# Kernel tuning notes

Measured on AMD Instinct MI355X. Metric: run time of the kernel, lower is better.

The kernel has to match this reference:

```python
import jax, jax.numpy as jnp
import numpy as np
import math

D_MODEL = 1024
N_HEADS = 16
D_K = D_MODEL // N_HEADS
NB_FEATURES = max(1, math.ceil(math.log(D_MODEL)))  # 7
D_FF = 4096
BH = 4  # block_size_h
BW = 4  # block_size_w
EPS_LN = 1e-6


def gelu_approx(x):
    c = math.sqrt(2.0 / math.pi)
    return 0.5 * x * (1.0 + jnp.tanh(c * (x + 0.044715 * x * x * x)))


def layer_norm(x, alpha, bias):
    # torch .std() uses ddof=1 (unbiased)
    mean = x.mean(axis=-1, keepdims=True)
    std = jnp.std(x, axis=-1, ddof=1, keepdims=True)
    return alpha * (x - mean) / (std + EPS_LN) + bias


def causal_performer(q_in, k_in, v_in, wq, wk, wv, wo, omega):
    B, Sq, D = q_in.shape
    Sk = k_in.shape[1]
    q = (q_in @ wq.T).reshape(B, Sq, N_HEADS, D_K)
    k = (k_in @ wk.T).reshape(B, Sk, N_HEADS, D_K)
    v = (v_in @ wv.T).reshape(B, Sk, N_HEADS, D_K)
    # exp kernel feature map: exp(-0.5 * (x @ omega^T)^2)
    qp = jnp.exp(-0.5 * jnp.square(q @ omega.T))  # (B,Sq,H,nb)
    kp = jnp.exp(-0.5 * jnp.square(k @ omega.T))  # (B,Sk,H,nb)
    qp = qp / (qp.sum(-1, keepdims=True) + 1e-6)
    kp = kp / (kp.sum(-1, keepdims=True) + 1e-6)
    K_cum = jnp.cumsum(kp, axis=1)                               # (B,Sk,H,nb)
    KV_cum = jnp.cumsum(kp[..., None] * v[..., None, :], axis=1)  # (B,Sk,H,nb,dk)
    key_idx = jnp.clip((jnp.arange(Sq) // BH + 1) * BW - 1, None, Sk - 1)
    K_sel = K_cum[:, key_idx]    # (B,Sq,H,nb)
    KV_sel = KV_cum[:, key_idx]  # (B,Sq,H,nb,dk)
    num = jnp.einsum('bshn,bshnd->bshd', qp, KV_sel)
    den = jnp.einsum('bshn,bshn->bsh', qp, K_sel)[..., None]
    out = (num / (den + 1e-6)).reshape(B, Sq, D)
    return out @ wo.T


def setup_inputs() -> dict:
    key = jax.random.key(0)
    ks = jax.random.split(key, 24)
    s = 0.02
    p = {}
    p['x'] = jax.random.normal(ks[0], (2, 4096, D_MODEL), jnp.float32)
    p['lto'] = jax.random.normal(ks[1], (2, 4096, D_MODEL), jnp.float32)
    for i, nm in enumerate(['wq_s', 'wk_s', 'wv_s', 'wo_s']):
        p[nm] = jax.random.normal(ks[2 + i], (D_MODEL, D_MODEL), jnp.float32) * s
    for i, nm in enumerate(['wq_c', 'wk_c', 'wv_c', 'wo_c']):
        p[nm] = jax.random.normal(ks[6 + i], (D_MODEL, D_MODEL), jnp.float32) * s
    p['omega_s'] = jax.random.normal(ks[10], (NB_FEATURES, D_K), jnp.float32) / math.sqrt(D_K)
    p['omega_c'] = jax.random.normal(ks[11], (NB_FEATURES, D_K), jnp.float32) / math.sqrt(D_K)
    p['w1'] = jax.random.normal(ks[12], (D_FF, D_MODEL), jnp.float32) * s
    p['b1'] = jnp.zeros((D_FF,), jnp.float32)
    p['w2'] = jax.random.normal(ks[13], (D_MODEL, D_FF), jnp.float32) * s
    p['b2'] = jnp.zeros((D_MODEL,), jnp.float32)
    for i in range(3):
        p[f'ln{i}_a'] = jnp.ones((D_MODEL,), jnp.float32)
        p[f'ln{i}_b'] = jnp.zeros((D_MODEL,), jnp.float32)
    return p


def reference(x, lto, wq_s, wk_s, wv_s, wo_s, wq_c, wk_c, wv_c, wo_c,
              omega_s, omega_c, w1, b1, w2, b2,
              ln0_a, ln0_b, ln1_a, ln1_b, ln2_a, ln2_b):
    # residual 0: self-attention on x
    xn = layer_norm(x, ln0_a, ln0_b)
    x = x + causal_performer(xn, xn, xn, wq_s, wk_s, wv_s, wo_s, omega_s)
    # residual 1: cross-attention, queries = normed lto, keys/values = updated x
    ln = layer_norm(lto, ln1_a, ln1_b)
    lto = lto + causal_performer(ln, x, x, wq_c, wk_c, wv_c, wo_c, omega_c)
    # residual 2: feed-forward
    fn = layer_norm(lto, ln2_a, ln2_b)
    ff = gelu_approx(fn @ w1.T + b1) @ w2.T + b2
    return lto + ff
```

## Files before the change

kernel.cpp:

```cpp
#include <hip/hip_runtime.h>
#include <cstdint>
#include <cstddef>

typedef __bf16 bf16;
typedef __bf16 bf16x8 __attribute__((ext_vector_type(8)));
typedef __bf16 bf16x4 __attribute__((ext_vector_type(4)));
typedef float  f32x4  __attribute__((ext_vector_type(4)));

#define NB 7
static constexpr int Bq = 2, Sq = 4096, Dm = 1024, Dff = 4096;
static constexpr int Mrows = Bq * Sq;
static constexpr int NCH = Sq / 4;
static constexpr int CSW = 464;

__device__ __forceinline__ void gload16(const void* g, void* l) {
  __builtin_amdgcn_global_load_lds((__attribute__((address_space(1))) void*)g,
                                   (__attribute__((address_space(3))) void*)l,
                                   16, 0, 0);
}

template <int N> __device__ __forceinline__ void wait_vmcnt() {
  asm volatile("s_waitcnt vmcnt(%0)" :: "n"(N) : "memory");
}
__device__ __forceinline__ void wait_lgkm0() {
  asm volatile("s_waitcnt lgkmcnt(0)" ::: "memory");
}
__device__ __forceinline__ void sbar() {
  __builtin_amdgcn_sched_barrier(0);
  __builtin_amdgcn_s_barrier();
  __builtin_amdgcn_sched_barrier(0);
}

__device__ __forceinline__ float gelu_f(float x) {
  const float c = 0.79788456080286535588f;
  float z = c * (x + 0.044715f * x * x * x);
  float t = 1.f - 2.f / (__expf(2.f * z) + 1.f);
  return 0.5f * x * (1.f + t);
}

struct CvtA {
  const float* s[10];
  bf16* d[10];
  int start[11];
};
__global__ __launch_bounds__(256) void cvt10(CvtA a) {
  const int i = blockIdx.x * 256 + threadIdx.x;
  int r = 0;
#pragma unroll
  for (int k = 1; k < 10; ++k) r += (i >= a.start[k]);
  const int o = i - a.start[r];
  f32x4 v = *(const f32x4*)&a.s[r][(size_t)o * 4];
  bf16x4 ov;
#pragma unroll
  for (int e = 0; e < 4; ++e) ov[e] = (bf16)v[e];
  *(bf16x4*)&a.d[r][(size_t)o * 4] = ov;
}

__global__ __launch_bounds__(256) void ln_kernel(const float* __restrict__ x,
                                                 const float* __restrict__ alpha,
                                                 const float* __restrict__ beta,
                                                 bf16* __restrict__ out) {
  const int row = blockIdx.x, tid = threadIdx.x;
  const float* xr = x + (size_t)row * Dm;
  f32x4 v = *(const f32x4*)&xr[tid * 4];
  float s  = v[0] + v[1] + v[2] + v[3];
  float s2 = v[0]*v[0] + v[1]*v[1] + v[2]*v[2] + v[3]*v[3];
#pragma unroll
  for (int o = 32; o > 0; o >>= 1) { s += __shfl_xor(s, o); s2 += __shfl_xor(s2, o); }
  __shared__ float red[8];
  const int wid = tid >> 6, lane = tid & 63;
  if (lane == 0) { red[wid] = s; red[wid + 4] = s2; }
  __syncthreads();
  s  = red[0] + red[1] + red[2] + red[3];
  s2 = red[4] + red[5] + red[6] + red[7];
  const float mean = s * (1.f / 1024.f);
  float var = (s2 - s * mean) * (1.f / 1023.f);
  var = fmaxf(var, 0.f);
  const float inv = 1.f / (sqrtf(var) + 1e-6f);
  f32x4 a4 = *(const f32x4*)&alpha[tid * 4];
  f32x4 b4 = *(const f32x4*)&beta[tid * 4];
  bf16x4 o4;
#pragma unroll
  for (int e = 0; e < 4; ++e) o4[e] = (bf16)(a4[e] * (v[e] - mean) * inv + b4[e]);
  *(bf16x4*)&out[(size_t)row * Dm + tid * 4] = o4;
}

template <int MODE>
__global__ __launch_bounds__(512, 2) void gemm256(
    const bf16* __restrict__ A, const bf16* __restrict__ Bw,
    int M, int N, int K,
    const float* __restrict__ bias, const float* __restrict__ res,
    float* __restrict__ outF, bf16* __restrict__ outB) {
  constexpr int BM = 256, BN = 256;
  constexpr int ACH = 4, LPT = 8, MFR = 8, MH = 4;
  __shared__ __align__(16) bf16 As[2][BM * 64];
  __shared__ __align__(16) bf16 Bs[2][BN * 64];

  const int tid = threadIdx.x;
  const int lane = tid & 63, wid = tid >> 6;
  const int wm = wid >> 2, wn = wid & 3;

  int bid = blockIdx.x;
  const int nwg = gridDim.x;
  bid = (bid & 7) * (nwg >> 3) + (bid >> 3);
  const int nbx = N / BN;
  const int bm = (bid / nbx) * BM, bn = (bid % nbx) * BN;
  const int NT = K >> 6;

  const int srow = tid >> 3;
  const int scol = ((tid & 7) ^ (srow & 7)) * 8;
  const bf16* Ag = A  + (size_t)(bm + srow) * K + scol;
  const bf16* Bg = Bw + (size_t)(bn + srow) * K + scol;

  f32x4 acc[MFR][4] = {};
  const int lr = lane & 15, uo = lane >> 4;

  auto stA = [&](int buf, int t) {
#pragma unroll
    for (int c = 0; c < ACH; ++c)
      gload16(Ag + ((size_t)(c * 64) * K + (size_t)t * 64),
              (char*)(&As[buf][0]) + c * 8192 + wid * 1024);
  };
  auto stB = [&](int buf, int t) {
#pragma unroll
    for (int c = 0; c < 4; ++c)
      gload16(Bg + ((size_t)(c * 64) * K + (size_t)t * 64),
              (char*)(&Bs[buf][0]) + c * 8192 + wid * 1024);
  };

  stA(0, 0); stB(0, 0);
  stA(1, 1); stB(1, 1);
  wait_vmcnt<LPT>();
  sbar();

  bf16x8 a0[MH][2], a1[MH][2], b0[2][2], b1[2][2];

  for (int t = 0; t < NT; ++t) {
    const int cur = t & 1;
    const bf16* Asb = &As[cur][0];
    const bf16* Bsb = &Bs[cur][0];

#pragma unroll
    for (int i = 0; i < MH; ++i)
#pragma unroll
      for (int kh = 0; kh < 2; ++kh) {
        const int r = wm * (BM / 2) + i * 16 + lr;
        const int u = (kh * 4 + uo) ^ (lr & 7);
        a0[i][kh] = *(const bf16x8*)&Asb[r * 64 + u * 8];
      }
#pragma unroll
    for (int j = 0; j < 2; ++j)
#pragma unroll
      for (int kh = 0; kh < 2; ++kh) {
        const int r = wn * 64 + j * 16 + lr;
        const int u = (kh * 4 + uo) ^ (lr & 7);
        b0[j][kh] = *(const bf16x8*)&Bsb[r * 64 + u * 8];
      }
    __builtin_amdgcn_sched_barrier(0);
    __builtin_amdgcn_s_barrier();
    wait_lgkm0();
    __builtin_amdgcn_sched_barrier(0);
    __builtin_amdgcn_s_setprio(1);
#pragma unroll
    for (int i = 0; i < MH; ++i)
#pragma unroll
      for (int j = 0; j < 2; ++j) {
        acc[i][j] = __builtin_amdgcn_mfma_f32_16x16x32_bf16(a0[i][0], b0[j][0], acc[i][j], 0, 0, 0);
        acc[i][j] = __builtin_amdgcn_mfma_f32_16x16x32_bf16(a0[i][1], b0[j][1], acc[i][j], 0, 0, 0);
      }
    __builtin_amdgcn_s_setprio(0);
    sbar();

#pragma unroll
    for (int j = 0; j < 2; ++j)
#pragma unroll
      for (int kh = 0; kh < 2; ++kh) {
        const int r = wn * 64 + (2 + j) * 16 + lr;
        const int u = (kh * 4 + uo) ^ (lr & 7);
        b1[j][kh] = *(const bf16x8*)&Bsb[r * 64 + u * 8];
      }
    __builtin_amdgcn_sched_barrier(0);
    __builtin_amdgcn_s_barrier();
    wait_lgkm0();
    __builtin_amdgcn_sched_barrier(0);
    __builtin_amdgcn_s_setprio(1);
#pragma unroll
    for (int i = 0; i < MH; ++i)
#pragma unroll
      for (int j = 0; j < 2; ++j) {
        acc[i][2 + j] = __builtin_amdgcn_mfma_f32_16x16x32_bf16(a0[i][0], b1[j][0], acc[i][2 + j], 0, 0, 0);
        acc[i][2 + j] = __builtin_amdgcn_mfma_f32_16x16x32_bf16(a0[i][1], b1[j][1], acc[i][2 + j], 0, 0, 0);
      }
    __builtin_amdgcn_s_setprio(0);
    sbar();

#pragma unroll
    for (int i = 0; i < MH; ++i)
#pragma unroll
      for (int kh = 0; kh < 2; ++kh) {
        const int r = wm * (BM / 2) + (MH + i) * 16 + lr;
        const int u = (kh * 4 + uo) ^ (lr & 7);
        a1[i][kh] = *(const bf16x8*)&Asb[r * 64 + u * 8];
      }
    __builtin_amdgcn_sched_barrier(0);
    if (t + 2 < NT) stB(cur, t + 2);
    __builtin_amdgcn_sched_barrier(0);
    __builtin_amdgcn_s_barrier();
    wait_lgkm0();
    __builtin_amdgcn_sched_barrier(0);
    __builtin_amdgcn_s_setprio(1);
#pragma unroll
    for (int i = 0; i < MH; ++i)
#pragma unroll
      for (int j = 0; j < 2; ++j) {
        acc[MH + i][2 + j] = __builtin_amdgcn_mfma_f32_16x16x32_bf16(a1[i][0], b1[j][0], acc[MH + i][2 + j], 0, 0, 0);
        acc[MH + i][2 + j] = __builtin_amdgcn_mfma_f32_16x16x32_bf16(a1[i][1], b1[j][1], acc[MH + i][2 + j], 0, 0, 0);
      }
    __builtin_amdgcn_s_setprio(0);
    sbar();

    if (t + 2 < NT) stA(cur, t + 2);
    __builtin_amdgcn_sched_barrier(0);
    __builtin_amdgcn_s_barrier();
    __builtin_amdgcn_sched_barrier(0);
    __builtin_amdgcn_s_setprio(1);
#pragma unroll
    for (int i = 0; i < MH; ++i)
#pragma unroll
      for (int j = 0; j < 2; ++j) {
        acc[MH + i][j] = __builtin_amdgcn_mfma_f32_16x16x32_bf16(a1[i][0], b0[j][0], acc[MH + i][j], 0, 0, 0);
        acc[MH + i][j] = __builtin_amdgcn_mfma_f32_16x16x32_bf16(a1[i][1], b0[j][1], acc[MH + i][j], 0, 0, 0);
      }
    __builtin_amdgcn_s_setprio(0);
    __builtin_amdgcn_sched_barrier(0);
    if (t < NT - 2) wait_vmcnt<LPT>();
    else            wait_vmcnt<0>();
    __builtin_amdgcn_s_barrier();
    __builtin_amdgcn_sched_barrier(0);
  }

#pragma unroll
  for (int f = 0; f < MFR; ++f) {
    const int r0 = bm + wm * (BM / 2) + f * 16 + (lane >> 4) * 4;
#pragma unroll
    for (int g = 0; g < 4; ++g) {
      const int c = bn + wn * 64 + g * 16 + (lane & 15);
      float bv = 0.f;
      if (MODE == 3) bv = bias[c];
#pragma unroll
      for (int r = 0; r < 4; ++r) {
        const size_t idx = (size_t)(r0 + r) * N + c;
        float v = acc[f][g][r];
        if (MODE == 3) v = gelu_f(v + bv);
        outB[idx] = (bf16)v;
      }
    }
  }
}

template <int MODE>
__global__ __launch_bounds__(512, 2) void gemm128(
    const bf16* __restrict__ A, const bf16* __restrict__ Bw,
    int M, int N, int K,
    const float* __restrict__ bias, const float* __restrict__ res,
    float* __restrict__ outF, bf16* __restrict__ outB) {
  constexpr int BM = 128, BN = 256;
  __shared__ __align__(16) bf16 As[3][BM * 64];
  __shared__ __align__(16) bf16 Bs[3][BN * 64];

  const int tid = threadIdx.x;
  const int lane = tid & 63, wid = tid >> 6;
  const int wm = wid >> 2, wn = wid & 3;

  int bid = blockIdx.x;
  const int nwg = gridDim.x;
  bid = (bid & 7) * (nwg >> 3) + (bid >> 3);
  const int nbx = N / BN;
  const int bm = (bid / nbx) * BM, bn = (bid % nbx) * BN;
  const int NT = K >> 6;

  const int srow = tid >> 3;
  const int scol = ((tid & 7) ^ (srow & 7)) * 8;
  const bf16* Ag = A  + (size_t)(bm + srow) * K + scol;
  const bf16* Bg = Bw + (size_t)(bn + srow) * K + scol;

  f32x4 acc[4][4] = {};
  const int lr = lane & 15, uo = lane >> 4;

  auto stA = [&](int buf, int t) {
#pragma unroll
    for (int c = 0; c < 2; ++c)
      gload16(Ag + ((size_t)(c * 64) * K + (size_t)t * 64),
              (char*)(&As[buf][0]) + c * 8192 + wid * 1024);
  };
  auto stB = [&](int buf, int t) {
#pragma unroll
    for (int c = 0; c < 4; ++c)
      gload16(Bg + ((size_t)(c * 64) * K + (size_t)t * 64),
              (char*)(&Bs[buf][0]) + c * 8192 + wid * 1024);
  };

  stA(0, 0); stB(0, 0);
  stA(1, 1); stB(1, 1);
  wait_vmcnt<6>();
  sbar();

  bf16x8 a0[2][2], a1[2][2], bv[4][2];
  int cur = 0;
  for (int t = 0; t < NT; ++t) {
    const bf16* Asb = &As[cur][0];
    const bf16* Bsb = &Bs[cur][0];
    const int nxt2 = (cur == 0) ? 2 : cur - 1;

#pragma unroll
    for (int i = 0; i < 2; ++i)
#pragma unroll
      for (int kh = 0; kh < 2; ++kh) {
        const int r = wm * 64 + i * 16 + lr;
        const int u = (kh * 4 + uo) ^ (lr & 7);
        a0[i][kh] = *(const bf16x8*)&Asb[r * 64 + u * 8];
      }
#pragma unroll
    for (int j = 0; j < 4; ++j)
#pragma unroll
      for (int kh = 0; kh < 2; ++kh) {
        const int r = wn * 64 + j * 16 + lr;
        const int u = (kh * 4 + uo) ^ (lr & 7);
        bv[j][kh] = *(const bf16x8*)&Bsb[r * 64 + u * 8];
      }
    __builtin_amdgcn_sched_barrier(0);
    if (t + 2 < NT) { stB(nxt2, t + 2); stA(nxt2, t + 2); }
    __builtin_amdgcn_sched_barrier(0);
    __builtin_amdgcn_s_barrier();
    wait_lgkm0();
    __builtin_amdgcn_sched_barrier(0);
    __builtin_amdgcn_s_setprio(1);
#pragma unroll
    for (int i = 0; i < 2; ++i)
#pragma unroll
      for (int j = 0; j < 4; ++j) {
        acc[i][j] = __builtin_amdgcn_mfma_f32_16x16x32_bf16(a0[i][0], bv[j][0], acc[i][j], 0, 0, 0);
        acc[i][j] = __builtin_amdgcn_mfma_f32_16x16x32_bf16(a0[i][1], bv[j][1], acc[i][j], 0, 0, 0);
      }
    __builtin_amdgcn_s_setprio(0);
    sbar();

#pragma unroll
    for (int i = 0; i < 2; ++i)
#pragma unroll
      for (int kh = 0; kh < 2; ++kh) {
        const int r = wm * 64 + (2 + i) * 16 + lr;
        const int u = (kh * 4 + uo) ^ (lr & 7);
        a1[i][kh] = *(const bf16x8*)&Asb[r * 64 + u * 8];
      }
    __builtin_amdgcn_sched_barrier(0);
    __builtin_amdgcn_s_barrier();
    wait_lgkm0();
    __builtin_amdgcn_sched_barrier(0);
    __builtin_amdgcn_s_setprio(1);
#pragma unroll
    for (int i = 0; i < 2; ++i)
#pragma unroll
      for (int j = 0; j < 4; ++j) {
        acc[2 + i][j] = __builtin_amdgcn_mfma_f32_16x16x32_bf16(a1[i][0], bv[j][0], acc[2 + i][j], 0, 0, 0);
        acc[2 + i][j] = __builtin_amdgcn_mfma_f32_16x16x32_bf16(a1[i][1], bv[j][1], acc[2 + i][j], 0, 0, 0);
      }
    __builtin_amdgcn_s_setprio(0);
    __builtin_amdgcn_sched_barrier(0);
    if (t < NT - 2) wait_vmcnt<6>();
    else            wait_vmcnt<0>();
    __builtin_amdgcn_s_barrier();
    __builtin_amdgcn_sched_barrier(0);
    cur = (cur == 2) ? 0 : cur + 1;
  }

#pragma unroll
  for (int f = 0; f < 4; ++f) {
    const int r0 = bm + wm * 64 + f * 16 + (lane >> 4) * 4;
#pragma unroll
    for (int g = 0; g < 4; ++g) {
      const int c = bn + wn * 64 + g * 16 + (lane & 15);
      float bvs = 0.f;
      if (MODE == 4) bvs = bias[c];
#pragma unroll
      for (int r = 0; r < 4; ++r) {
        const size_t idx = (size_t)(r0 + r) * N + c;
        float v = acc[f][g][r];
        if (MODE == 1 || MODE == 2) v += res[idx];
        if (MODE == 4) v += bvs + res[idx];
        if (MODE == 0 || MODE == 1) outB[idx] = (bf16)v;
        else outF[idx] = v;
      }
    }
  }
}

__global__ __launch_bounds__(512) void perf_cs(
    const bf16* __restrict__ kmat, const bf16* __restrict__ vmat, int ld,
    const float* __restrict__ omega, float* __restrict__ CS,
    float* __restrict__ segtot) {
  const int tid = threadIdx.x;
  const int bh = blockIdx.y, b = bh >> 4, h = bh & 15;
  const int seg = blockIdx.x;
  const int s0 = seg * 512;
  __shared__ __align__(16) bf16 vs[512][64];
  __shared__ float kps[512][8];
  __shared__ float oms[448];

  {
    const bf16* vb = vmat + ((size_t)(b * Sq + s0)) * ld + h * 64;
#pragma unroll
    for (int p = 0; p < 8; ++p) {
      const int row = p * 64 + (tid >> 3), c16 = (tid & 7) * 8;
      *(uint4*)&vs[row][c16 ^ ((row & 7) * 8)] =
          *(const uint4*)&vb[(size_t)row * ld + c16];
    }
  }
  if (tid < 448) oms[tid] = omega[tid];
  __syncthreads();

  {
    const int row = tid;
    const bf16* kr = kmat + ((size_t)(b * Sq + s0 + row)) * ld + h * 64;
    bf16x8 kv[8];
#pragma unroll
    for (int q = 0; q < 8; ++q) kv[q] = *(const bf16x8*)&kr[q * 8];
    float f[NB];
#pragma unroll
    for (int n = 0; n < NB; ++n) f[n] = 0.f;
#pragma unroll
    for (int d = 0; d < 64; ++d) {
      const float kd = (float)kv[d >> 3][d & 7];
#pragma unroll
      for (int n = 0; n < NB; ++n) f[n] += kd * oms[n * 64 + d];
    }
    float sum = 1e-6f, e[NB];
#pragma unroll
    for (int n = 0; n < NB; ++n) { e[n] = __expf(-0.5f * f[n] * f[n]); sum += e[n]; }
    const float inv = 1.f / sum;
#pragma unroll
    for (int n = 0; n < NB; ++n) kps[row][n] = e[n] * inv;
    kps[row][7] = 0.f;
  }
  __syncthreads();

  if (tid < CSW) {
    const int comp = tid;
    float* outb = CS + ((size_t)bh * NCH + seg * 128) * CSW;
    float r = 0.f;
    if (comp < 8) {
      for (int c = 0; c < 128; ++c) {
        if (comp < 7)
          r += kps[4*c][comp] + kps[4*c+1][comp] + kps[4*c+2][comp] + kps[4*c+3][comp];
        outb[(size_t)c * CSW + comp] = r;
      }
    } else if (comp < 456) {
      const int n = (comp - 8) >> 6, d = (comp - 8) & 63;
      for (int c = 0; c < 128; ++c) {
#pragma unroll
        for (int i = 0; i < 4; ++i) {
          const int row = 4 * c + i;
          r += kps[row][n] * (float)vs[row][d ^ ((row & 7) * 8)];
        }
        outb[(size_t)c * CSW + comp] = r;
      }
    } else {
      for (int c = 0; c < 128; ++c) outb[(size_t)c * CSW + comp] = 0.f;
    }
    segtot[((size_t)bh * 8 + seg) * CSW + comp] = r;
  }
}

__global__ __launch_bounds__(256) void perf_scan2(float* __restrict__ segtot) {
  const int bh = blockIdx.x;
  const int c0 = threadIdx.x;
  float run0 = 0.f, run1 = 0.f;
#pragma unroll
  for (int s = 0; s < 8; ++s) {
    float* st = segtot + ((size_t)bh * 8 + s) * CSW;
    float t0 = st[c0]; st[c0] = run0; run0 += t0;
    if (c0 + 256 < CSW) { float t1 = st[c0 + 256]; st[c0 + 256] = run1; run1 += t1; }
  }
}

__global__ __launch_bounds__(256) void perf_out(
    const bf16* __restrict__ qmat, int ldq, const float* __restrict__ omega,
    const float* __restrict__ CS, const float* __restrict__ segtot,
    bf16* __restrict__ attn) {
  const int tid = threadIdx.x;
  const int bh = blockIdx.y, b = bh >> 4, h = bh & 15;
  const int s0 = blockIdx.x * 128;
  const int cg0 = s0 >> 2;
  const int seg = cg0 >> 7;
  __shared__ __align__(16) float Ps[32 * CSW];
  __shared__ float qps[128][8];
  __shared__ float oms[NB * 64];

  {
    const float* src = CS + ((size_t)bh * NCH + cg0) * CSW;
    const float* off = segtot + ((size_t)bh * 8 + seg) * CSW;
    for (int i = tid; i < 32 * CSW / 4; i += 256) {
      f32x4 a = *(const f32x4*)&src[i * 4];
      f32x4 o = *(const f32x4*)&off[(i % (CSW / 4)) * 4];
      a += o;
      *(f32x4*)&Ps[i * 4] = a;
    }
  }
  if (tid < 224) { oms[tid] = omega[tid]; oms[tid + 224] = omega[tid + 224]; }
  __syncthreads();
  {
    const int p = tid >> 1, half = tid & 1;
    const bf16* qr = qmat + ((size_t)(b * Sq + s0 + p)) * ldq + h * 64 + half * 32;
    bf16x8 qv[4];
#pragma unroll
    for (int q = 0; q < 4; ++q) qv[q] = *(const bf16x8*)&qr[q * 8];
    float f[NB];
#pragma unroll
    for (int n = 0; n < NB; ++n) f[n] = 0.f;
#pragma unroll
    for (int d = 0; d < 32; ++d) {
      float qd = (float)qv[d >> 3][d & 7];
#pragma unroll
      for (int n = 0; n < NB; ++n) f[n] += qd * oms[n * 64 + half * 32 + d];
    }
    float sum = 1e-6f;
    float e[NB];
#pragma unroll
    for (int n = 0; n < NB; ++n) {
      float full = f[n] + __shfl_xor(f[n], 1);
      e[n] = __expf(-0.5f * full * full);
      sum += e[n];
    }
    float inv = 1.f / sum;
    if (half == 0) {
      float den = 1e-6f;
      const float* Pr = &Ps[(p >> 2) * CSW];
#pragma unroll
      for (int n = 0; n < NB; ++n) {
        float qn = e[n] * inv;
        qps[p][n] = qn;
        den += qn * Pr[n];
      }
      qps[p][7] = 1.f / den;
    }
  }
  __syncthreads();
  {
    const int d = tid & 63, w = tid >> 6;
    for (int qq = w; qq < 128; qq += 4) {
      const float* Pr = &Ps[(qq >> 2) * CSW + 8 + d];
      float num = 0.f;
#pragma unroll
      for (int n = 0; n < NB; ++n) num += qps[qq][n] * Pr[n * 64];
      attn[((size_t)(b * Sq + s0 + qq)) * Dm + h * 64 + d] = (bf16)(num * qps[qq][7]);
    }
  }
}

extern "C" void kernel_launch(void* const* d_in, const int* in_sizes, int n_in,
                              void* d_out, int out_size, void* d_ws, size_t ws_size,
                              hipStream_t stream) {
  const float* x    = (const float*)d_in[0];
  const float* lto  = (const float*)d_in[1];
  const float* w_s[4] = {(const float*)d_in[2], (const float*)d_in[3],
                         (const float*)d_in[4], (const float*)d_in[5]};
  const float* w_c[4] = {(const float*)d_in[6], (const float*)d_in[7],
                         (const float*)d_in[8], (const float*)d_in[9]};
  const float* omega_s = (const float*)d_in[10];
  const float* omega_c = (const float*)d_in[11];
  const float* w1 = (const float*)d_in[12];
  const float* b1 = (const float*)d_in[13];
  const float* w2 = (const float*)d_in[14];
  const float* b2 = (const float*)d_in[15];
  const float* ln_a[3] = {(const float*)d_in[16], (const float*)d_in[18], (const float*)d_in[20]};
  const float* ln_b[3] = {(const float*)d_in[17], (const float*)d_in[19], (const float*)d_in[21]};

  char* ws = (char*)d_ws;
  size_t off = 0;
  auto alloc = [&](size_t bytes) -> char* {
    char* p = ws + off;
    off += (bytes + 255) & ~(size_t)255;
    return p;
  };

  const size_t actB = (size_t)Mrows * Dm * sizeof(bf16);
  const size_t MB32 = (size_t)Mrows * 2048 * sizeof(bf16);

  bf16* wqkv = (bf16*)alloc((size_t)3072 * 1024 * 2);
  bf16* wo_sb = (bf16*)alloc((size_t)1024 * 1024 * 2);
  bf16* wq_cb = (bf16*)alloc((size_t)1024 * 1024 * 2);
  bf16* wkv  = (bf16*)alloc((size_t)2048 * 1024 * 2);
  bf16* wo_cb = (bf16*)alloc((size_t)1024 * 1024 * 2);
  bf16* w1b = (bf16*)alloc((size_t)Dff * Dm * 2);
  bf16* w2b = (bf16*)alloc((size_t)Dff * Dm * 2);
  bf16* xnb  = (bf16*)alloc(actB);
  char* pool = alloc((size_t)Mrows * Dff * 2);
  bf16* qkvb = (bf16*)pool;
  bf16* kvb  = (bf16*)pool;
  bf16* qb   = (bf16*)(pool + MB32);
  bf16* hb   = (bf16*)pool;
  bf16* attnb= (bf16*)alloc(actB);
  bf16* x2b  = (bf16*)alloc(actB);
  bf16* ln1b = (bf16*)alloc(actB);
  float* lto2 = (float*)alloc((size_t)Mrows * Dm * 4);
  float* CSb  = (float*)alloc((size_t)32 * NCH * CSW * 4);
  float* stb  = (float*)alloc((size_t)32 * 8 * CSW * 4);
  bf16* fnb = xnb;

  {
    CvtA a;
    const float* srcs[10] = {w_s[0], w_s[1], w_s[2], w_s[3], w_c[0],
                             w_c[1], w_c[2], w_c[3], w1, w2};
    bf16* dsts[10] = {wqkv, wqkv + 1048576, wqkv + 2097152, wo_sb, wq_cb,
                      wkv, wkv + 1048576, wo_cb, w1b, w2b};
    const int SM = 262144, LG = 1048576;
    int st = 0;
    for (int i = 0; i < 10; ++i) {
      a.s[i] = srcs[i]; a.d[i] = dsts[i]; a.start[i] = st;
      st += (i < 8) ? SM : LG;
    }
    a.start[10] = st;
    cvt10<<<st / 256, 256, 0, stream>>>(a);
  }

  dim3 gperf(Sq / 128, Bq * 16);
  dim3 gseg(8, Bq * 16);
  const int gQKV = (Mrows / 256) * (3072 / 256);
  const int gKV  = (Mrows / 256) * (2048 / 256);
  const int gFF1 = (Mrows / 256) * (4096 / 256);
  const int gN1k = (Mrows / 128) * (1024 / 256);

  ln_kernel<<<Mrows, 256, 0, stream>>>(x, ln_a[0], ln_b[0], xnb);
  gemm256<0><<<gQKV, 512, 0, stream>>>(xnb, wqkv, Mrows, 3072, 1024, nullptr, nullptr, nullptr, qkvb);
  perf_cs<<<gseg, 512, 0, stream>>>(qkvb + 1024, qkvb + 2048, 3072, omega_s, CSb, stb);
  perf_scan2<<<32, 256, 0, stream>>>(stb);
  perf_out<<<gperf, 256, 0, stream>>>(qkvb, 3072, omega_s, CSb, stb, attnb);
  gemm128<1><<<gN1k, 512, 0, stream>>>(attnb, wo_sb, Mrows, 1024, 1024, nullptr, x, nullptr, x2b);

  ln_kernel<<<Mrows, 256, 0, stream>>>(lto, ln_a[1], ln_b[1], ln1b);
  gemm128<0><<<gN1k, 512, 0, stream>>>(ln1b, wq_cb, Mrows, 1024, 1024, nullptr, nullptr, nullptr, qb);
  gemm256<0><<<gKV, 512, 0, stream>>>(x2b, wkv, Mrows, 2048, 1024, nullptr, nullptr, nullptr, kvb);
  perf_cs<<<gseg, 512, 0, stream>>>(kvb, kvb + 1024, 2048, omega_c, CSb, stb);
  perf_scan2<<<32, 256, 0, stream>>>(stb);
  perf_out<<<gperf, 256, 0, stream>>>(qb, 1024, omega_c, CSb, stb, attnb);
  gemm128<2><<<gN1k, 512, 0, stream>>>(attnb, wo_cb, Mrows, 1024, 1024, nullptr, lto, lto2, nullptr);

  ln_kernel<<<Mrows, 256, 0, stream>>>(lto2, ln_a[2], ln_b[2], fnb);
  gemm256<3><<<gFF1, 512, 0, stream>>>(fnb, w1b, Mrows, 4096, 1024, b1, nullptr, nullptr, hb);
  gemm128<4><<<gN1k, 512, 0, stream>>>(hb, w2b, Mrows, 1024, 4096, b2, lto2, (float*)d_out, nullptr);
}
```

Measured before the change: 596.8 us.

## Replace 256-tile GEMMs with a single simpler 128x128 double-buffered GEMM kernel

Removes the 256x256 and 128x256 GEMM kernels, whose multi-phase interleaved LDS-read/MFMA schedules used 512 threads and triple buffering. All GEMMs now use one 128x128 tile kernel with 256 threads (4 waves, 64x64 each), simple double buffering, and a single load-then-compute phase per k-step. The epilogue modes are merged so GELU+bias is handled in this kernel too. The smaller tiles give more blocks and less LDS per block, but lower data reuse per tile and drop the fine-grained overlap of LDS reads with MFMA work.

```diff
diff --git a/kernel.cpp b/kernel.cpp
--- a/kernel.cpp
+++ b/kernel.cpp
@@ -24,11 +24,6 @@
 }
 __device__ __forceinline__ void wait_lgkm0() {
   asm volatile("s_waitcnt lgkmcnt(0)" ::: "memory");
-}
-__device__ __forceinline__ void sbar() {
-  __builtin_amdgcn_sched_barrier(0);
-  __builtin_amdgcn_s_barrier();
-  __builtin_amdgcn_sched_barrier(0);
 }
 
 __device__ __forceinline__ float gelu_f(float x) {
@@ -86,19 +81,18 @@
 }
 
 template <int MODE>
-__global__ __launch_bounds__(512, 2) void gemm256(
+__global__ __launch_bounds__(256, 2) void gemm128(
     const bf16* __restrict__ A, const bf16* __restrict__ Bw,
     int M, int N, int K,
     const float* __restrict__ bias, const float* __restrict__ res,
     float* __restrict__ outF, bf16* __restrict__ outB) {
-  constexpr int BM = 256, BN = 256;
-  constexpr int ACH = 4, LPT = 8, MFR = 8, MH = 4;
+  constexpr int BM = 128, BN = 128;
   __shared__ __align__(16) bf16 As[2][BM * 64];
   __shared__ __align__(16) bf16 Bs[2][BN * 64];
 
   const int tid = threadIdx.x;
   const int lane = tid & 63, wid = tid >> 6;
-  const int wm = wid >> 2, wn = wid & 3;
+  const int wm = wid >> 1, wn = wid & 1;
 
   int bid = blockIdx.x;
   const int nwg = gridDim.x;
@@ -112,28 +106,28 @@
   const bf16* Ag = A  + (size_t)(bm + srow) * K + scol;
   const bf16* Bg = Bw + (size_t)(bn + srow) * K + scol;
 
-  f32x4 acc[MFR][4] = {};
+  f32x4 acc[4][4] = {};
   const int lr = lane & 15, uo = lane >> 4;
 
   auto stA = [&](int buf, int t) {
 #pragma unroll
-    for (int c = 0; c < ACH; ++c)
-      gload16(Ag + ((size_t)(c * 64) * K + (size_t)t * 64),
-              (char*)(&As[buf][0]) + c * 8192 + wid * 1024);
+    for (int c = 0; c < 4; ++c)
+      gload16(Ag + ((size_t)(c * 32) * K + (size_t)t * 64),
+              (char*)(&As[buf][0]) + c * 4096 + wid * 1024);
   };
   auto stB = [&](int buf, int t) {
 #pragma unroll
     for (int c = 0; c < 4; ++c)
-      gload16(Bg + ((size_t)(c * 64) * K + (size_t)t * 64),
-              (char*)(&Bs[buf][0]) + c * 8192 + wid * 1024);
+      gload16(Bg + ((size_t)(c * 32) * K + (size_t)t * 64),
+              (char*)(&Bs[buf][0]) + c * 4096 + wid * 1024);
   };
 
   stA(0, 0); stB(0, 0);
   stA(1, 1); stB(1, 1);
-  wait_vmcnt<LPT>();
-  sbar();
-
-  bf16x8 a0[MH][2], a1[MH][2], b0[2][2], b1[2][2];
+  wait_vmcnt<8>();
+  __builtin_amdgcn_s_barrier();
+
+  bf16x8 a[4][2], b[4][2];
 
   for (int t = 0; t < NT; ++t) {
     const int cur = t & 1;
@@ -141,254 +135,62 @@
     const bf16* Bsb = &Bs[cur][0];
 
 #pragma unroll
-    for (int i = 0; i < MH; ++i)
+    for (int i = 0; i < 4; ++i)
 #pragma unroll
       for (int kh = 0; kh < 2; ++kh) {
-        const int r = wm * (BM / 2) + i * 16 + lr;
+        const int r = wm * 64 + i * 16 + lr;
         const int u = (kh * 4 + uo) ^ (lr & 7);
-        a0[i][kh] = *(const bf16x8*)&Asb[r * 64 + u * 8];
-      }
-#pragma unroll
-    for (int j = 0; j < 2; ++j)
+        a[i][kh] = *(const bf16x8*)&Asb[r * 64 + u * 8];
+      }
+#pragma unroll
+    for (int j = 0; j < 4; ++j)
 #pragma unroll
       for (int kh = 0; kh < 2; ++kh) {
         const int r = wn * 64 + j * 16 + lr;
         const int u = (kh * 4 + uo) ^ (lr & 7);
-        b0[j][kh] = *(const bf16x8*)&Bsb[r * 64 + u * 8];
-      }
-    __builtin_amdgcn_sched_barrier(0);
-    __builtin_amdgcn_s_barrier();
+        b[j][kh] = *(const bf16x8*)&Bsb[r * 64 + u * 8];
+      }
     wait_lgkm0();
-    __builtin_amdgcn_sched_barrier(0);
-    __builtin_amdgcn_s_setprio(1);
-#pragma unroll
-    for (int i = 0; i < MH; ++i)
-#pragma unroll
-      for (int j = 0; j < 2; ++j) {
-        acc[i][j] = __builtin_amdgcn_mfma_f32_16x16x32_bf16(a0[i][0], b0[j][0], acc[i][j], 0, 0, 0);
-        acc[i][j] = __builtin_amdgcn_mfma_f32_16x16x32_bf16(a0[i][1], b0[j][1], acc[i][j], 0, 0, 0);
-      }
-    __builtin_amdgcn_s_setprio(0);
-    sbar();
-
-#pragma unroll
-    for (int j = 0; j < 2; ++j)
-#pragma unroll
-      for (int kh = 0; kh < 2; ++kh) {
-        const int r = wn * 64 + (2 + j) * 16 + lr;
-        const int u = (kh * 4 + uo) ^ (lr & 7);
-        b1[j][kh] = *(const bf16x8*)&Bsb[r * 64 + u * 8];
-      }
-    __builtin_amdgcn_sched_barrier(0);
-    __builtin_amdgcn_s_barrier();
-    wait_lgkm0();
-    __builtin_amdgcn_sched_barrier(0);
-    __builtin_amdgcn_s_setprio(1);
-#pragma unroll
-    for (int i = 0; i < MH; ++i)
-#pragma unroll
-      for (int j = 0; j < 2; ++j) {
-        acc[i][2 + j] = __builtin_amdgcn_mfma_f32_16x16x32_bf16(a0[i][0], b1[j][0], acc[i][2 + j], 0, 0, 0);
-        acc[i][2 + j] = __builtin_amdgcn_mfma_f32_16x16x32_bf16(a0[i][1], b1[j][1], acc[i][2 + j], 0, 0, 0);
-      }
-    __builtin_amdgcn_s_setprio(0);
-    sbar();
-
-#pragma unroll
-    for (int i = 0; i < MH; ++i)
-#pragma unroll
-      for (int kh = 0; kh < 2; ++kh) {
-        const int r = wm * (BM / 2) + (MH + i) * 16 + lr;
-        const int u = (kh * 4 + uo) ^ (lr & 7);
-        a1[i][kh] = *(const bf16x8*)&Asb[r * 64 + u * 8];
-      }
-    __builtin_amdgcn_sched_barrier(0);
-    if (t + 2 < NT) stB(cur, t + 2);
-    __builtin_amdgcn_sched_barrier(0);
-    __builtin_amdgcn_s_barrier();
-    wait_lgkm0();
-    __builtin_amdgcn_sched_barrier(0);
-    __builtin_amdgcn_s_setprio(1);
-#pragma unroll
-    for (int i = 0; i < MH; ++i)
-#pragma unroll
-      for (int j = 0; j < 2; ++j) {
-        acc[MH + i][2 + j] = __builtin_amdgcn_mfma_f32_16x16x32_bf16(a1[i][0], b1[j][0], acc[MH + i][2 + j], 0, 0, 0);
-        acc[MH + i][2 + j] = __builtin_amdgcn_mfma_f32_16x16x32_bf16(a1[i][1], b1[j][1], acc[MH + i][2 + j], 0, 0, 0);
-      }
-    __builtin_amdgcn_s_setprio(0);
-    sbar();
-
-    if (t + 2 < NT) stA(cur, t + 2);
     __builtin_amdgcn_sched_barrier(0);
     __builtin_amdgcn_s_barrier();
     __builtin_amdgcn_sched_barrier(0);
+
+    if (t + 2 < NT) { stA(cur, t + 2); stB(cur, t + 2); }
+    __builtin_amdgcn_sched_barrier(0);
+
     __builtin_amdgcn_s_setprio(1);
 #pragma unroll
-    for (int i = 0; i < MH; ++i)
-#pragma unroll
-      for (int j = 0; j < 2; ++j) {
-        acc[MH + i][j] = __builtin_amdgcn_mfma_f32_16x16x32_bf16(a1[i][0], b0[j][0], acc[MH + i][j], 0, 0, 0);
-        acc[MH + i][j] = __builtin_amdgcn_mfma_f32_16x16x32_bf16(a1[i][1], b0[j][1], acc[MH + i][j], 0, 0, 0);
+    for (int i = 0; i < 4; ++i)
+#pragma unroll
+      for (int j = 0; j < 4; ++j) {
+        acc[i][j] = __builtin_amdgcn_mfma_f32_16x16x32_bf16(a[i][0], b[j][0], acc[i][j], 0, 0, 0);
+        acc[i][j] = __builtin_amdgcn_mfma_f32_16x16x32_bf16(a[i][1], b[j][1], acc[i][j], 0, 0, 0);
       }
     __builtin_amdgcn_s_setprio(0);
     __builtin_amdgcn_sched_barrier(0);
-    if (t < NT - 2) wait_vmcnt<LPT>();
+
+    if (t < NT - 2) wait_vmcnt<8>();
     else            wait_vmcnt<0>();
     __builtin_amdgcn_s_barrier();
     __builtin_amdgcn_sched_barrier(0);
   }
 
 #pragma unroll
-  for (int f = 0; f < MFR; ++f) {
-    const int r0 = bm + wm * (BM / 2) + f * 16 + (lane >> 4) * 4;
+  for (int f = 0; f < 4; ++f) {
+    const int r0 = bm + wm * 64 + f * 16 + (lane >> 4) * 4;
 #pragma unroll
     for (int g = 0; g < 4; ++g) {
       const int c = bn + wn * 64 + g * 16 + (lane & 15);
       float bv = 0.f;
-      if (MODE == 3) bv = bias[c];
-#pragma unroll
-      for (int r = 0; r < 4; ++r) {
-        const size_t idx = (size_t)(r0 + r) * N + c;
-        float v = acc[f][g][r];
-        if (MODE == 3) v = gelu_f(v + bv);
-        outB[idx] = (bf16)v;
-      }
-    }
-  }
-}
-
-template <int MODE>
-__global__ __launch_bounds__(512, 2) void gemm128(
-    const bf16* __restrict__ A, const bf16* __restrict__ Bw,
-    int M, int N, int K,
-    const float* __restrict__ bias, const float* __restrict__ res,
-    float* __restrict__ outF, bf16* __restrict__ outB) {
-  constexpr int BM = 128, BN = 256;
-  __shared__ __align__(16) bf16 As[3][BM * 64];
-  __shared__ __align__(16) bf16 Bs[3][BN * 64];
-
-  const int tid = threadIdx.x;
-  const int lane = tid & 63, wid = tid >> 6;
-  const int wm = wid >> 2, wn = wid & 3;
-
-  int bid = blockIdx.x;
-  const int nwg = gridDim.x;
-  bid = (bid & 7) * (nwg >> 3) + (bid >> 3);
-  const int nbx = N / BN;
-  const int bm = (bid / nbx) * BM, bn = (bid % nbx) * BN;
-  const int NT = K >> 6;
-
-  const int srow = tid >> 3;
-  const int scol = ((tid & 7) ^ (srow & 7)) * 8;
-  const bf16* Ag = A  + (size_t)(bm + srow) * K + scol;
-  const bf16* Bg = Bw + (size_t)(bn + srow) * K + scol;
-
-  f32x4 acc[4][4] = {};
-  const int lr = lane & 15, uo = lane >> 4;
-
-  auto stA = [&](int buf, int t) {
-#pragma unroll
-    for (int c = 0; c < 2; ++c)
-      gload16(Ag + ((size_t)(c * 64) * K + (size_t)t * 64),
-              (char*)(&As[buf][0]) + c * 8192 + wid * 1024);
-  };
-  auto stB = [&](int buf, int t) {
-#pragma unroll
-    for (int c = 0; c < 4; ++c)
-      gload16(Bg + ((size_t)(c * 64) * K + (size_t)t * 64),
-              (char*)(&Bs[buf][0]) + c * 8192 + wid * 1024);
-  };
-
-  stA(0, 0); stB(0, 0);
-  stA(1, 1); stB(1, 1);
-  wait_vmcnt<6>();
-  sbar();
-
-  bf16x8 a0[2][2], a1[2][2], bv[4][2];
-  int cur = 0;
-  for (int t = 0; t < NT; ++t) {
-    const bf16* Asb = &As[cur][0];
-    const bf16* Bsb = &Bs[cur][0];
-    const int nxt2 = (cur == 0) ? 2 : cur - 1;
-
-#pragma unroll
-    for (int i = 0; i < 2; ++i)
-#pragma unroll
-      for (int kh = 0; kh < 2; ++kh) {
-        const int r = wm * 64 + i * 16 + lr;
-        const int u = (kh * 4 + uo) ^ (lr & 7);
-        a0[i][kh] = *(const bf16x8*)&Asb[r * 64 + u * 8];
-      }
-#pragma unroll
-    for (int j = 0; j < 4; ++j)
-#pragma unroll
-      for (int kh = 0; kh < 2; ++kh) {
-        const int r = wn * 64 + j * 16 + lr;
-        const int u = (kh * 4 + uo) ^ (lr & 7);
-        bv[j][kh] = *(const bf16x8*)&Bsb[r * 64 + u * 8];
-      }
-    __builtin_amdgcn_sched_barrier(0);
-    if (t + 2 < NT) { stB(nxt2, t + 2); stA(nxt2, t + 2); }
-    __builtin_amdgcn_sched_barrier(0);
-    __builtin_amdgcn_s_barrier();
-    wait_lgkm0();
-    __builtin_amdgcn_sched_barrier(0);
-    __builtin_amdgcn_s_setprio(1);
-#pragma unroll
-    for (int i = 0; i < 2; ++i)
-#pragma unroll
-      for (int j = 0; j < 4; ++j) {
-        acc[i][j] = __builtin_amdgcn_mfma_f32_16x16x32_bf16(a0[i][0], bv[j][0], acc[i][j], 0, 0, 0);
-        acc[i][j] = __builtin_amdgcn_mfma_f32_16x16x32_bf16(a0[i][1], bv[j][1], acc[i][j], 0, 0, 0);
-      }
-    __builtin_amdgcn_s_setprio(0);
-    sbar();
-
-#pragma unroll
-    for (int i = 0; i < 2; ++i)
-#pragma unroll
-      for (int kh = 0; kh < 2; ++kh) {
-        const int r = wm * 64 + (2 + i) * 16 + lr;
-        const int u = (kh * 4 + uo) ^ (lr & 7);
-        a1[i][kh] = *(const bf16x8*)&Asb[r * 64 + u * 8];
-      }
-    __builtin_amdgcn_sched_barrier(0);
-    __builtin_amdgcn_s_barrier();
-    wait_lgkm0();
-    __builtin_amdgcn_sched_barrier(0);
-    __builtin_amdgcn_s_setprio(1);
-#pragma unroll
-    for (int i = 0; i < 2; ++i)
-#pragma unroll
-      for (int j = 0; j < 4; ++j) {
-        acc[2 + i][j] = __builtin_amdgcn_mfma_f32_16x16x32_bf16(a1[i][0], bv[j][0], acc[2 + i][j], 0, 0, 0);
-        acc[2 + i][j] = __builtin_amdgcn_mfma_f32_16x16x32_bf16(a1[i][1], bv[j][1], acc[2 + i][j], 0, 0, 0);
-      }
-    __builtin_amdgcn_s_setprio(0);
-    __builtin_amdgcn_sched_barrier(0);
-    if (t < NT - 2) wait_vmcnt<6>();
-    else            wait_vmcnt<0>();
-    __builtin_amdgcn_s_barrier();
-    __builtin_amdgcn_sched_barrier(0);
-    cur = (cur == 2) ? 0 : cur + 1;
-  }
-
-#pragma unroll
-  for (int f = 0; f < 4; ++f) {
-    const int r0 = bm + wm * 64 + f * 16 + (lane >> 4) * 4;
-#pragma unroll
-    for (int g = 0; g < 4; ++g) {
-      const int c = bn + wn * 64 + g * 16 + (lane & 15);
-      float bvs = 0.f;
-      if (MODE == 4) bvs = bias[c];
+      if (MODE == 3 || MODE == 4) bv = bias[c];
 #pragma unroll
       for (int r = 0; r < 4; ++r) {
         const size_t idx = (size_t)(r0 + r) * N + c;
         float v = acc[f][g][r];
         if (MODE == 1 || MODE == 2) v += res[idx];
-        if (MODE == 4) v += bvs + res[idx];
-        if (MODE == 0 || MODE == 1) outB[idx] = (bf16)v;
+        if (MODE == 3) v = gelu_f(v + bv);
+        if (MODE == 4) v += bv + res[idx];
+        if (MODE == 0 || MODE == 1 || MODE == 3) outB[idx] = (bf16)v;
         else outF[idx] = v;
       }
     }
@@ -625,27 +427,27 @@
 
   dim3 gperf(Sq / 128, Bq * 16);
   dim3 gseg(8, Bq * 16);
-  const int gQKV = (Mrows / 256) * (3072 / 256);
-  const int gKV  = (Mrows / 256) * (2048 / 256);
-  const int gFF1 = (Mrows / 256) * (4096 / 256);
-  const int gN1k = (Mrows / 128) * (1024 / 256);
+  const int gQKV = (Mrows / 128) * (3072 / 128);
+  const int gKV  = (Mrows / 128) * (2048 / 128);
+  const int gFF1 = (Mrows / 128) * (4096 / 128);
+  const int gN1k = (Mrows / 128) * (1024 / 128);
 
   ln_kernel<<<Mrows, 256, 0, stream>>>(x, ln_a[0], ln_b[0], xnb);
-  gemm256<0><<<gQKV, 512, 0, stream>>>(xnb, wqkv, Mrows, 3072, 1024, nullptr, nullptr, nullptr, qkvb);
+  gemm128<0><<<gQKV, 256, 0, stream>>>(xnb, wqkv, Mrows, 3072, 1024, nullptr, nullptr, nullptr, qkvb);
   perf_cs<<<gseg, 512, 0, stream>>>(qkvb + 1024, qkvb + 2048, 3072, omega_s, CSb, stb);
   perf_scan2<<<32, 256, 0, stream>>>(stb);
   perf_out<<<gperf, 256, 0, stream>>>(qkvb, 3072, omega_s, CSb, stb, attnb);
-  gemm128<1><<<gN1k, 512, 0, stream>>>(attnb, wo_sb, Mrows, 1024, 1024, nullptr, x, nullptr, x2b);
+  gemm128<1><<<gN1k, 256, 0, stream>>>(attnb, wo_sb, Mrows, 1024, 1024, nullptr, x, nullptr, x2b);
 
   ln_kernel<<<Mrows, 256, 0, stream>>>(lto, ln_a[1], ln_b[1], ln1b);
-  gemm128<0><<<gN1k, 512, 0, stream>>>(ln1b, wq_cb, Mrows, 1024, 1024, nullptr, nullptr, nullptr, qb);
-  gemm256<0><<<gKV, 512, 0, stream>>>(x2b, wkv, Mrows, 2048, 1024, nullptr, nullptr, nullptr, kvb);
+  gemm128<0><<<gN1k, 256, 0, stream>>>(ln1b, wq_cb, Mrows, 1024, 1024, nullptr, nullptr, nullptr, qb);
+  gemm128<0><<<gKV, 256, 0, stream>>>(x2b, wkv, Mrows, 2048, 1024, nullptr, nullptr, nullptr, kvb);
   perf_cs<<<gseg, 512, 0, stream>>>(kvb, kvb + 1024, 2048, omega_c, CSb, stb);
   perf_scan2<<<32, 256, 0, stream>>>(stb);
   perf_out<<<gperf, 256, 0, stream>>>(qb, 1024, omega_c, CSb, stb, attnb);
-  gemm128<2><<<gN1k, 512, 0, stream>>>(attnb, wo_cb, Mrows, 1024, 1024, nullptr, lto, lto2, nullptr);
+  gemm128<2><<<gN1k, 256, 0, stream>>>(attnb, wo_cb, Mrows, 1024, 1024, nullptr, lto, lto2, nullptr);
 
   ln_kernel<<<Mrows, 256, 0, stream>>>(lto2, ln_a[2], ln_b[2], fnb);
-  gemm256<3><<<gFF1, 512, 0, stream>>>(fnb, w1b, Mrows, 4096, 1024, b1, nullptr, nullptr, hb);
-  gemm128<4><<<gN1k, 512, 0, stream>>>(hb, w2b, Mrows, 1024, 4096, b2, lto2, (float*)d_out, nullptr);
-}
+  gemm128<3><<<gFF1, 256, 0, stream>>>(fnb, w1b, Mrows, 4096, 1024, b1, nullptr, nullptr, hb);
+  gemm128<4><<<gN1k, 256, 0, stream>>>(hb, w2b, Mrows, 1024, 4096, b2, lto2, (float*)d_out, nullptr);
+}
```

New measurement: 533.2 us. 10.7% less time.
